# Optimization experiments

Measured on AMD Instinct MI355X. Metric: run time of the kernel, lower is better.

## Reference

```python
import jax, jax.numpy as jnp
import numpy as np

B, S, N, NODE_IN, IN_DIM, H, EMB = 2048, 168, 64, 16, 16, 64, 4
# N == H is required by the original broadcast `attention_score * station_features_emb`


def setup_inputs() -> dict:
    key = jax.random.key(0)
    ks = jax.random.split(key, 24)
    p = lambda i, shape, s=0.05: jax.random.normal(ks[i], shape, jnp.float32) * s
    inp = {
        "local_node": jax.random.normal(ks[0], (B, NODE_IN), jnp.float32),
        "station_nodes": jax.random.normal(ks[1], (B, N, NODE_IN), jnp.float32),
        "station_features": jax.random.normal(ks[2], (B, S, IN_DIM), jnp.float32),
    }
    weather = jax.random.randint(ks[3], (B, S, 1), 0, 12)
    wind = jax.random.randint(ks[4], (B, S, 1), 0, 10)
    month = jax.random.randint(ks[5], (B, S, 1), 1, 13)  # 1-indexed in source
    day = jax.random.randint(ks[6], (B, S, 1), 1, 8)
    hour = jax.random.randint(ks[7], (B, S, 1), 1, 25)
    inp["station_emb"] = jnp.stack([weather, wind, month, day, hour], axis=-1).astype(jnp.int32)  # (B,S,1,5)
    inp.update(
        emb_weather=p(8, (12, EMB), 1.0), emb_wind=p(9, (10, EMB), 1.0),
        emb_month=p(10, (12, EMB), 1.0), emb_day=p(11, (7, EMB), 1.0),
        emb_hour=p(12, (24, EMB), 1.0),
        W_nodes=p(13, (H, NODE_IN)), b_nodes=jnp.zeros((H,), jnp.float32),
        W_attn=p(14, (1, 2 * H)), b_attn=jnp.zeros((1,), jnp.float32),
        W_d1=p(15, (H // 2, IN_DIM + 5 * EMB)), b_d1=jnp.zeros((H // 2,), jnp.float32),
        W_d2=p(16, (H, H // 2)), b_d2=jnp.zeros((H,), jnp.float32),
        Wih0=p(17, (3 * H, 2 * H)), Whh0=p(18, (3 * H, H)),
        bih0=jnp.zeros((3 * H,), jnp.float32), bhh0=jnp.zeros((3 * H,), jnp.float32),
        Wih1=p(19, (3 * H, H)), Whh1=p(20, (3 * H, H)),
        bih1=jnp.zeros((3 * H,), jnp.float32), bhh1=jnp.zeros((3 * H,), jnp.float32),
        W_pred=p(21, (1, 2 * H)), b_pred=jnp.zeros((1,), jnp.float32),
    )
    return inp


def _gru_layer(x, Wih, Whh, bih, bhh):
    # x: (B,S,Din); PyTorch GRU gate math, gates ordered (r,z,n).
    xg = jnp.einsum('bsd,gd->sbg', x, Wih) + bih  # (S,B,3H) precomputed input gates
    h0 = jnp.zeros((x.shape[0], Whh.shape[1]), x.dtype)

    def step(h, xg_t):
        gh = h @ Whh.T + bhh
        xr, xz, xn = jnp.split(xg_t, 3, axis=-1)
        hr, hz, hn = jnp.split(gh, 3, axis=-1)
        r = jax.nn.sigmoid(xr + hr)
        z = jax.nn.sigmoid(xz + hz)
        n = jnp.tanh(xn + r * hn)
        h_new = (1.0 - z) * n + z * h
        return h_new, h_new

    h_last, hs = jax.lax.scan(step, h0, xg)
    return jnp.swapaxes(hs, 0, 1), h_last  # (B,S,H), (B,H)


def _forward(local_node, station_nodes, station_features, station_emb,
             emb_weather, emb_wind, emb_month, emb_day, emb_hour,
             W_nodes, b_nodes, W_attn, b_attn, W_d1, b_d1, W_d2, b_d2,
             Wih0, Whh0, bih0, bhh0, Wih1, Whh1, bih1, bhh1, W_pred, b_pred):
    local_emb = jnp.tanh(local_node @ W_nodes.T + b_nodes)          # (B,H)
    site_emb = jnp.tanh(station_nodes @ W_nodes.T + b_nodes)        # (B,N,H)
    # attn(cat(local, site)) == local@Wl + site@Ws + b, vectorized over sites
    Wl, Ws = W_attn[0, :H], W_attn[0, H:]
    energies = site_emb @ Ws + (local_emb @ Wl)[:, None] + b_attn[0]  # (B,N)
    attn = jax.nn.softmax(energies, axis=-1)                          # (B,N), N==H

    e = lambda tab, idx: tab[idx].reshape(idx.shape[0], idx.shape[1], -1)  # (B,S,EMB)
    cat = jnp.concatenate([
        station_features,
        e(emb_weather, station_emb[..., 0]),
        e(emb_wind, station_emb[..., 1]),
        e(emb_month, station_emb[..., 2] - 1),
        e(emb_day, station_emb[..., 3] - 1),
        e(emb_hour, station_emb[..., 4] - 1),
    ], axis=-1)                                                      # (B,S,IN_DIM+20)
    h1 = jnp.tanh(cat @ W_d1.T + b_d1)
    sfe = jnp.tanh(h1 @ W_d2.T + b_d2)                               # (B,S,H)

    local_feature = attn[:, None, :] * sfe                           # broadcast over seq
    features = jnp.concatenate([local_feature, sfe], axis=-1)        # (B,S,2H)

    out0, hf0 = _gru_layer(features, Wih0, Whh0, bih0, bhh0)
    out1, hf1 = _gru_layer(out0, Wih1, Whh1, bih1, bhh1)
    hidden = jnp.concatenate([hf0, hf1], axis=-1)                    # (B,2H)
    pred = jnp.tanh(hidden @ W_pred.T + b_pred)                      # (B,1)
    return pred


def reference(local_node, station_nodes, station_features, station_emb,
              emb_weather, emb_wind, emb_month, emb_day, emb_hour,
              W_nodes, b_nodes, W_attn, b_attn, W_d1, b_d1, W_d2, b_d2,
              Wih0, Whh0, bih0, bhh0, Wih1, Whh1, bih1, bhh1, W_pred, b_pred):
    return _forward(local_node, station_nodes, station_features, station_emb,
                    emb_weather, emb_wind, emb_month, emb_day, emb_hour,
                    W_nodes, b_nodes, W_attn, b_attn, W_d1, b_d1, W_d2, b_d2,
                    Wih0, Whh0, bih0, bhh0, Wih1, Whh1, bih1, bhh1, W_pred, b_pred)
```

## Files before the change

### kernel.cpp

```cpp
#include <hip/hip_runtime.h>
#include <cstdint>
#include <cstddef>

#define B_ 2048
#define S_ 168
#define NT_ 5376

typedef _Float16 h2_t __attribute__((ext_vector_type(2)));
typedef _Float16 f16x8 __attribute__((ext_vector_type(8)));
typedef float f32x4 __attribute__((ext_vector_type(4)));
typedef unsigned int u32;

__device__ __forceinline__ unsigned pack_h2f(float a, float b){
    h2_t v; v.x = (_Float16)a; v.y = (_Float16)b;
    return __builtin_bit_cast(unsigned, v);
}
__device__ __forceinline__ float fast_exp(float x){
    return __builtin_amdgcn_exp2f(x * 1.44269504088896340736f);
}
__device__ __forceinline__ float fast_sigmoid(float x){
    return __builtin_amdgcn_rcpf(1.0f + fast_exp(-x));
}
__device__ __forceinline__ float fast_tanh(float x){
    return 1.0f - 2.0f * __builtin_amdgcn_rcpf(1.0f + fast_exp(2.0f * x));
}
__device__ __forceinline__ void wsync(){
    asm volatile("s_waitcnt lgkmcnt(0)" ::: "memory");
    __builtin_amdgcn_wave_barrier();
}
__device__ __forceinline__ void bar_lds(){
    asm volatile("s_waitcnt lgkmcnt(0)\n\ts_barrier" ::: "memory");
}
__device__ __forceinline__ f32x4 mfma16(uint4 a, uint4 b, f32x4 c){
    return __builtin_amdgcn_mfma_f32_16x16x32_f16(
        __builtin_bit_cast(f16x8, a), __builtin_bit_cast(f16x8, b), c, 0, 0, 0);
}
__device__ __forceinline__ uint4 load_bfrag(const float* __restrict__ W, int ldk,
                                            int o, int kk0, int kmax){
    float w[8];
    #pragma unroll
    for (int e = 0; e < 8; ++e){
        int kk = kk0 + e;
        w[e] = (kk < kmax) ? W[o*ldk + kk] : 0.f;
    }
    uint4 r;
    r.x = pack_h2f(w[0], w[1]); r.y = pack_h2f(w[2], w[3]);
    r.z = pack_h2f(w[4], w[5]); r.w = pack_h2f(w[6], w[7]);
    return r;
}

__global__ void nbst_attn(const float* __restrict__ sn, const float* __restrict__ Wn,
                          const float* __restrict__ bn, const float* __restrict__ Wa,
                          float* __restrict__ attnO){
    __shared__ float WnL[64*16];
    __shared__ float WsL[64];
    __shared__ float bnL[64];
    const int tid = threadIdx.x;
    for (int e = tid; e < 1024; e += 256) WnL[e] = Wn[e];
    if (tid < 64){ WsL[tid] = Wa[64 + tid]; bnL[tid] = bn[tid]; }
    __syncthreads();
    const int wv = tid >> 6, l = tid & 63;
    const int b = blockIdx.x * 4 + wv;
    const float* xp = sn + ((size_t)b * 64 + l) * 16;
    float x[16];
    #pragma unroll
    for (int k = 0; k < 16; ++k) x[k] = xp[k];
    float e_i = 0.f;
    for (int h = 0; h < 64; ++h){
        float acc = bnL[h];
        #pragma unroll
        for (int k = 0; k < 16; ++k) acc += x[k] * WnL[h*16 + k];
        e_i += fast_tanh(acc) * WsL[h];
    }
    float m = e_i;
    #pragma unroll
    for (int s = 32; s >= 1; s >>= 1) m = fmaxf(m, __shfl_xor(m, s));
    float p = fast_exp(e_i - m);
    float ssum = p;
    #pragma unroll
    for (int s = 32; s >= 1; s >>= 1) ssum += __shfl_xor(ssum, s);
    attnO[(size_t)b*64 + l] = p * __builtin_amdgcn_rcpf(ssum);
}

#define A0_CAT 0
#define A0_H1  2304
#define A0_FT  3584
#define A0_WM  7936
#define A0_EMB 9984
#define A0_ATT 10244
#define A0_TOT 11268

__global__ __launch_bounds__(256, 2)
void nbst_mlpxg0(const float* __restrict__ sf, const int* __restrict__ se,
                 const float* __restrict__ e0, const float* __restrict__ e1,
                 const float* __restrict__ e2, const float* __restrict__ e3,
                 const float* __restrict__ e4,
                 const float* __restrict__ Wd1, const float* __restrict__ bd1,
                 const float* __restrict__ Wd2, const float* __restrict__ bd2,
                 const float* __restrict__ Wih0, const float* __restrict__ attnI,
                 u32* __restrict__ xg0F)
{
    __shared__ u32 sm[A0_TOT];
    float* smF = reinterpret_cast<float*>(sm);
    const int tid = threadIdx.x;
    const int w = tid >> 6, l = tid & 63;
    const int q = l >> 4, c = l & 15;

    for (int e = tid; e < 260; e += 256){
        float v;
        if (e < 48)       v = e0[e];
        else if (e < 88)  v = e1[e-48];
        else if (e < 136) v = e2[e-88];
        else if (e < 164) v = e3[e-136];
        else              v = e4[e-164];
        smF[A0_EMB + e] = v;
    }
    for (int f = w; f < 8; f += 4){
        uint4 fr;
        if (f < 4){ int n = f >> 1, ks = f & 1;
                    fr = load_bfrag(Wd1, 36, 16*n + c, 32*ks + 8*q, 36); }
        else      { int n = f - 4;
                    fr = load_bfrag(Wd2, 32, 16*n + c, 8*q, 32); }
        *reinterpret_cast<uint4*>(sm + A0_WM + (f*64 + l)*4) = fr;
    }
    uint4 bw[3][4];
    #pragma unroll
    for (int nn = 0; nn < 3; ++nn)
        #pragma unroll
        for (int ks = 0; ks < 4; ++ks)
            bw[nn][ks] = load_bfrag(Wih0, 128, 16*(w + 4*nn) + c, 32*ks + 8*q, 128);
    for (int e = tid; e < 64*18; e += 256){
        int row = e / 18, j = 18 + e % 18;
        sm[A0_CAT + row*36 + j] = 0u;
    }
    const float bb10 = bd1[c],  bb11 = bd1[16+c];
    const float bb20 = bd2[c],  bb21 = bd2[16+c];
    const float bb22 = bd2[32+c], bb23 = bd2[48+c];
    __syncthreads();

    for (int tile = blockIdx.x; tile < NT_; tile += gridDim.x){
        const int gb = tile / 42, tb = tile % 42;
        for (int e = tid; e < 1024; e += 256)
            smF[A0_ATT + e] = attnI[(size_t)(16*gb)*64 + e];
        for (int e = tid; e < 64*18; e += 256){
            int row = e / 18, j = e % 18;
            int R = (16*gb + (row & 15))*S_ + 4*tb + (row >> 4);
            float c0, c1;
            if (j < 8){
                c0 = sf[(size_t)R*16 + 2*j]; c1 = sf[(size_t)R*16 + 2*j + 1];
            } else {
                int jj = j - 8, ebl = jj >> 1, d0 = (jj & 1) * 2;
                int idx = se[(size_t)R*5 + ebl] - (ebl >= 2 ? 1 : 0);
                const int toff = (ebl==0)?0:(ebl==1)?48:(ebl==2)?88:(ebl==3)?136:164;
                c0 = smF[A0_EMB + toff + idx*4 + d0];
                c1 = smF[A0_EMB + toff + idx*4 + d0 + 1];
            }
            sm[A0_CAT + row*36 + j] = pack_h2f(c0, c1);
        }
        __syncthreads();

        {
            f32x4 c1a[2];
            c1a[0] = (f32x4){bb10, bb10, bb10, bb10};
            c1a[1] = (f32x4){bb11, bb11, bb11, bb11};
            #pragma unroll
            for (int ks = 0; ks < 2; ++ks){
                uint4 a = *reinterpret_cast<const uint4*>(
                    sm + A0_CAT + (16*w + c)*36 + ks*16 + 4*q);
                #pragma unroll
                for (int n = 0; n < 2; ++n)
                    c1a[n] = mfma16(a, *reinterpret_cast<const uint4*>(
                        sm + A0_WM + ((n*2 + ks)*64 + l)*4), c1a[n]);
            }
            #pragma unroll
            for (int n = 0; n < 2; ++n)
                #pragma unroll
                for (int j = 0; j < 4; ++j){
                    float v = fast_tanh(c1a[n][j]);
                    float vp = __shfl_xor(v, 1);
                    if (!(l & 1))
                        sm[A0_H1 + (16*w + 4*q + j)*20 + 8*n + (c >> 1)] = pack_h2f(v, vp);
                }
        }
        wsync();

        {
            uint4 a = *reinterpret_cast<const uint4*>(
                sm + A0_H1 + (16*w + c)*20 + 4*q);
            f32x4 c2[4];
            c2[0] = (f32x4){bb20, bb20, bb20, bb20};
            c2[1] = (f32x4){bb21, bb21, bb21, bb21};
            c2[2] = (f32x4){bb22, bb22, bb22, bb22};
            c2[3] = (f32x4){bb23, bb23, bb23, bb23};
            #pragma unroll
            for (int n = 0; n < 4; ++n)
                c2[n] = mfma16(a, *reinterpret_cast<const uint4*>(
                    sm + A0_WM + ((4 + n)*64 + l)*4), c2[n]);
            #pragma unroll
            for (int n = 0; n < 4; ++n)
                #pragma unroll
                for (int j = 0; j < 4; ++j){
                    float s  = fast_tanh(c2[n][j]);
                    float fa = smF[A0_ATT + (4*q + j)*64 + 16*n + c] * s;
                    float sp  = __shfl_xor(s, 1);
                    float fap = __shfl_xor(fa, 1);
                    if (!(l & 1)){
                        int row = 16*w + 4*q + j;
                        int ci = 8*n + (c >> 1);
                        sm[A0_FT + row*68 + ci]      = pack_h2f(fa, fap);
                        sm[A0_FT + row*68 + 32 + ci] = pack_h2f(s, sp);
                    }
                }
        }
        __syncthreads();

        #pragma unroll
        for (int m = 0; m < 4; ++m){
            uint4 af[4];
            #pragma unroll
            for (int ks = 0; ks < 4; ++ks)
                af[ks] = *reinterpret_cast<const uint4*>(
                    sm + A0_FT + (16*m + c)*68 + ks*16 + 4*q);
            f32x4 acc[3];
            #pragma unroll
            for (int nn = 0; nn < 3; ++nn) acc[nn] = (f32x4){0.f, 0.f, 0.f, 0.f};
            #pragma unroll
            for (int ks = 0; ks < 4; ++ks)
                #pragma unroll
                for (int nn = 0; nn < 3; ++nn)
                    acc[nn] = mfma16(af[ks], bw[nn][ks], acc[nn]);
            size_t base = ((size_t)(gb*S_ + 4*tb + m))*1536 + (size_t)w*384 + (size_t)l*6;
            uint2 s01, s23, s45;
            s01.x = pack_h2f(acc[0][0], acc[0][1]); s01.y = pack_h2f(acc[0][2], acc[0][3]);
            s23.x = pack_h2f(acc[1][0], acc[1][1]); s23.y = pack_h2f(acc[1][2], acc[1][3]);
            s45.x = pack_h2f(acc[2][0], acc[2][1]); s45.y = pack_h2f(acc[2][2], acc[2][3]);
            *reinterpret_cast<uint2*>(xg0F + base + 0) = s01;
            *reinterpret_cast<uint2*>(xg0F + base + 2) = s23;
            *reinterpret_cast<uint2*>(xg0F + base + 4) = s45;
        }
        __syncthreads();
    }
}

#define RW0 6912
#define RW1 13056
#define RHB (RW0 + RW1)
#define RF_TOT (RHB + 2048)

__global__ __launch_bounds__(512, 1)
void nbst_recf(const u32* __restrict__ xg0F,
               const float* __restrict__ Whh0,
               const float* __restrict__ bih0, const float* __restrict__ bhh0,
               const float* __restrict__ Wih1, const float* __restrict__ Whh1,
               const float* __restrict__ bih1, const float* __restrict__ bhh1,
               const float* __restrict__ Wpred, const float* __restrict__ bpred,
               float* __restrict__ outp)
{
    extern __shared__ u32 sm[];
    u32* smw0 = sm;
    u32* smw1 = sm + RW0;
    u32* HB0  = sm + RHB;
    u32* HB1  = sm + RHB + 1024;
    const int tid = threadIdx.x;
    const int w8 = tid >> 6, l = tid & 63;
    const int grp = w8 >> 2, w = w8 & 3;
    const int q = l >> 4, c = l & 15;
    const int g = blockIdx.x, B0 = g*16;

    for (int e = tid; e < 192*32; e += 512){
        int row = e >> 5, k = e & 31;
        smw0[row*36 + k] = pack_h2f(Whh0[row*64 + 2*k], Whh0[row*64 + 2*k + 1]);
    }
    for (int e = tid; e < 192*64; e += 512){
        int row = e / 64, kp = e % 64;
        smw1[row*68 + kp] = (kp < 32)
            ? pack_h2f(Wih1[row*64 + 2*kp],      Wih1[row*64 + 2*kp + 1])
            : pack_h2f(Whh1[row*64 + 2*(kp-32)], Whh1[row*64 + 2*(kp-32) + 1]);
    }
    for (int e = tid; e < 2048; e += 512) sm[RHB + e] = 0u;
    __syncthreads();

    const int gr = 16*w + c, gz = 64 + 16*w + c, gn = 128 + 16*w + c;
    const int rd0 = (c*32 + 4*q)      ^ ((c & 7) << 2);
    const int rd1 = (c*32 + 4*q + 16) ^ ((c & 7) << 2);
    int wri[4];
    #pragma unroll
    for (int j = 0; j < 4; ++j){
        int row = 4*q + j;
        wri[j] = (row*64 + 16*w + c) ^ ((row & 7) << 3);
    }

    float hv0 = 0.f, hv1 = 0.f, hv2 = 0.f, hv3 = 0.f;

    if (grp == 0){
        uint4 aBR[2], aBZ[2], aBHN[2];
        #pragma unroll
        for (int ks = 0; ks < 2; ++ks){
            aBR[ks]  = *reinterpret_cast<const uint4*>(smw0 + gr*36 + 16*ks + 4*q);
            aBZ[ks]  = *reinterpret_cast<const uint4*>(smw0 + gz*36 + 16*ks + 4*q);
            aBHN[ks] = *reinterpret_cast<const uint4*>(smw0 + gn*36 + 16*ks + 4*q);
        }
        const float br0 = bih0[gr] + bhh0[gr], bz0 = bih0[gz] + bhh0[gz];
        const float bxn0 = bih0[gn], bhn0 = bhh0[gn];

        const u32* xb = xg0F + (size_t)g * S_ * 1536 + (size_t)w * 384 + (size_t)l * 6;
        uint2 x0a, x0b, x0c, x1a, x1b, x1c, x2a, x2b, x2c, x3a, x3b, x3c;
        {
            const u32* p0 = xb;
            const u32* p1 = xb + 1536;
            const u32* p2 = xb + 2*1536;
            const u32* p3 = xb + 3*1536;
            x0a = *(const uint2*)(p0+0); x0b = *(const uint2*)(p0+2); x0c = *(const uint2*)(p0+4);
            x1a = *(const uint2*)(p1+0); x1b = *(const uint2*)(p1+2); x1c = *(const uint2*)(p1+4);
            x2a = *(const uint2*)(p2+0); x2b = *(const uint2*)(p2+2); x2c = *(const uint2*)(p2+4);
            x3a = *(const uint2*)(p3+0); x3b = *(const uint2*)(p3+2); x3c = *(const uint2*)(p3+4);
        }

#define L0STEP(I, XA, XB, XC) do{                                               \
    const int i_ = (I);                                                         \
    const u32* hp0_ = HB0 + ((i_ + 1) & 1) * 512;                               \
    uint4 hA0a_ = *(const uint4*)(hp0_ + rd0);                                  \
    uint4 hA0b_ = *(const uint4*)(hp0_ + rd1);                                  \
    f32x4 aRh_ = {br0,br0,br0,br0};                                             \
    f32x4 aZh_ = {bz0,bz0,bz0,bz0};                                             \
    f32x4 aHN_ = {bhn0,bhn0,bhn0,bhn0};                                         \
    aRh_ = mfma16(hA0a_, aBR[0], aRh_);  aRh_ = mfma16(hA0b_, aBR[1], aRh_);    \
    aZh_ = mfma16(hA0a_, aBZ[0], aZh_);  aZh_ = mfma16(hA0b_, aBZ[1], aZh_);    \
    aHN_ = mfma16(hA0a_, aBHN[0], aHN_); aHN_ = mfma16(hA0b_, aBHN[1], aHN_);   \
    h2_t xR01_ = __builtin_bit_cast(h2_t, (XA).x);                              \
    h2_t xR23_ = __builtin_bit_cast(h2_t, (XA).y);                              \
    h2_t xZ01_ = __builtin_bit_cast(h2_t, (XB).x);                              \
    h2_t xZ23_ = __builtin_bit_cast(h2_t, (XB).y);                              \
    h2_t xN01_ = __builtin_bit_cast(h2_t, (XC).x);                              \
    h2_t xN23_ = __builtin_bit_cast(h2_t, (XC).y);                              \
    _Float16* hw_ = (_Float16*)(HB0 + (i_ & 1) * 512);                          \
    float rg_, zg_, ng_;                                                        \
    rg_ = fast_sigmoid((float)xR01_.x + aRh_[0]);                               \
    zg_ = fast_sigmoid((float)xZ01_.x + aZh_[0]);                               \
    ng_ = fast_tanh((float)xN01_.x + bxn0 + rg_*aHN_[0]);                       \
    hv0 = (1.f - zg_)*ng_ + zg_*hv0; hw_[wri[0]] = (_Float16)hv0;               \
    rg_ = fast_sigmoid((float)xR01_.y + aRh_[1]);                               \
    zg_ = fast_sigmoid((float)xZ01_.y + aZh_[1]);                               \
    ng_ = fast_tanh((float)xN01_.y + bxn0 + rg_*aHN_[1]);                       \
    hv1 = (1.f - zg_)*ng_ + zg_*hv1; hw_[wri[1]] = (_Float16)hv1;               \
    rg_ = fast_sigmoid((float)xR23_.x + aRh_[2]);                               \
    zg_ = fast_sigmoid((float)xZ23_.x + aZh_[2]);                               \
    ng_ = fast_tanh((float)xN23_.x + bxn0 + rg_*aHN_[2]);                       \
    hv2 = (1.f - zg_)*ng_ + zg_*hv2; hw_[wri[2]] = (_Float16)hv2;               \
    rg_ = fast_sigmoid((float)xR23_.y + aRh_[3]);                               \
    zg_ = fast_sigmoid((float)xZ23_.y + aZh_[3]);                               \
    ng_ = fast_tanh((float)xN23_.y + bxn0 + rg_*aHN_[3]);                       \
    hv3 = (1.f - zg_)*ng_ + zg_*hv3; hw_[wri[3]] = (_Float16)hv3;               \
    {   int tn_ = (i_ + 4 < S_) ? i_ + 4 : S_ - 1;                              \
        const u32* xp_ = xb + (size_t)tn_ * 1536;                               \
        (XA) = *(const uint2*)(xp_ + 0);                                        \
        (XB) = *(const uint2*)(xp_ + 2);                                        \
        (XC) = *(const uint2*)(xp_ + 4);                                        \
    }                                                                           \
    bar_lds();                                                                  \
} while(0)

        L0STEP(0, x0a, x0b, x0c);
        L0STEP(1, x1a, x1b, x1c);
        L0STEP(2, x2a, x2b, x2c);
        L0STEP(3, x3a, x3b, x3c);
        #pragma unroll 1
        for (int i4 = 1; i4 < 42; ++i4){
            const int ib = 4*i4;
            L0STEP(ib + 0, x0a, x0b, x0c);
            L0STEP(ib + 1, x1a, x1b, x1c);
            L0STEP(ib + 2, x2a, x2b, x2c);
            L0STEP(ib + 3, x3a, x3b, x3c);
        }
        bar_lds();
#undef L0STEP
    } else {
        uint4 xBR[2], xBZ[2], xBXN[2], hBR[2], hBZ[2], hBHN[2];
        #pragma unroll
        for (int ks = 0; ks < 2; ++ks){
            xBR[ks] = *reinterpret_cast<const uint4*>(smw1 + gr*68 + 16*ks + 4*q);
            xBZ[ks] = *reinterpret_cast<const uint4*>(smw1 + gz*68 + 16*ks + 4*q);
            hBR[ks] = *reinterpret_cast<const uint4*>(smw1 + gr*68 + 32 + 16*ks + 4*q);
            hBZ[ks] = *reinterpret_cast<const uint4*>(smw1 + gz*68 + 32 + 16*ks + 4*q);
        }
        xBXN[0] = *reinterpret_cast<const uint4*>(smw1 + gn*68 +      4*q);
        xBXN[1] = *reinterpret_cast<const uint4*>(smw1 + gn*68 + 16 + 4*q);
        hBHN[0] = *reinterpret_cast<const uint4*>(smw1 + gn*68 + 32 + 4*q);
        hBHN[1] = *reinterpret_cast<const uint4*>(smw1 + gn*68 + 48 + 4*q);
        const float br1 = bih1[gr] + bhh1[gr], bz1 = bih1[gz] + bhh1[gz];
        const float bxn1 = bih1[gn], bhn1 = bhh1[gn];

        bar_lds();
        #pragma unroll 1
        for (int i = 1; i <= S_; ++i){
            const u32* hp0_ = HB0 + ((i + 1) & 1) * 512;
            const u32* hp1_ = HB1 + ((i + 1) & 1) * 512;
            uint4 hA0a_ = *(const uint4*)(hp0_ + rd0);
            uint4 hA0b_ = *(const uint4*)(hp0_ + rd1);
            uint4 hA1a_ = *(const uint4*)(hp1_ + rd0);
            uint4 hA1b_ = *(const uint4*)(hp1_ + rd1);
            f32x4 cR_  = {br1,br1,br1,br1};
            f32x4 cZ_  = {bz1,bz1,bz1,bz1};
            f32x4 cXN_ = {bxn1,bxn1,bxn1,bxn1};
            f32x4 cHN_ = {bhn1,bhn1,bhn1,bhn1};
            cR_  = mfma16(hA0a_, xBR[0], cR_);   cR_  = mfma16(hA0b_, xBR[1], cR_);
            cZ_  = mfma16(hA0a_, xBZ[0], cZ_);   cZ_  = mfma16(hA0b_, xBZ[1], cZ_);
            cXN_ = mfma16(hA0a_, xBXN[0], cXN_); cXN_ = mfma16(hA0b_, xBXN[1], cXN_);
            cR_  = mfma16(hA1a_, hBR[0], cR_);   cR_  = mfma16(hA1b_, hBR[1], cR_);
            cZ_  = mfma16(hA1a_, hBZ[0], cZ_);   cZ_  = mfma16(hA1b_, hBZ[1], cZ_);
            cHN_ = mfma16(hA1a_, hBHN[0], cHN_); cHN_ = mfma16(hA1b_, hBHN[1], cHN_);
            _Float16* hw_ = (_Float16*)(HB1 + (i & 1) * 512);
            float rg_, zg_, ng_;
            rg_ = fast_sigmoid(cR_[0]); zg_ = fast_sigmoid(cZ_[0]);
            ng_ = fast_tanh(cXN_[0] + rg_*cHN_[0]);
            hv0 = (1.f - zg_)*ng_ + zg_*hv0; hw_[wri[0]] = (_Float16)hv0;
            rg_ = fast_sigmoid(cR_[1]); zg_ = fast_sigmoid(cZ_[1]);
            ng_ = fast_tanh(cXN_[1] + rg_*cHN_[1]);
            hv1 = (1.f - zg_)*ng_ + zg_*hv1; hw_[wri[1]] = (_Float16)hv1;
            rg_ = fast_sigmoid(cR_[2]); zg_ = fast_sigmoid(cZ_[2]);
            ng_ = fast_tanh(cXN_[2] + rg_*cHN_[2]);
            hv2 = (1.f - zg_)*ng_ + zg_*hv2; hw_[wri[2]] = (_Float16)hv2;
            rg_ = fast_sigmoid(cR_[3]); zg_ = fast_sigmoid(cZ_[3]);
            ng_ = fast_tanh(cXN_[3] + rg_*cHN_[3]);
            hv3 = (1.f - zg_)*ng_ + zg_*hv3; hw_[wri[3]] = (_Float16)hv3;
            bar_lds();
        }
    }

    __syncthreads();
    float* s0 = reinterpret_cast<float*>(sm);
    float* s1 = reinterpret_cast<float*>(sm) + 1024;
    {
        float* sd = (grp == 0) ? s0 : s1;
        #pragma unroll
        for (int j = 0; j < 4; ++j){
            int row = 4*q + j;
            float hv = (j == 0) ? hv0 : (j == 1) ? hv1 : (j == 2) ? hv2 : hv3;
            sd[row*64 + 16*w + c] = hv;
        }
    }
    __syncthreads();
    if (tid < 256){
        const int r = tid >> 4, cg = tid & 15;
        const float* hp0 = s0 + r*64 + 4*cg;
        const float* hp1 = s1 + r*64 + 4*cg;
        const float* wp0 = Wpred + 4*cg;
        const float* wp1 = Wpred + 64 + 4*cg;
        float part = hp0[0]*wp0[0] + hp0[1]*wp0[1] + hp0[2]*wp0[2] + hp0[3]*wp0[3]
                   + hp1[0]*wp1[0] + hp1[1]*wp1[1] + hp1[2]*wp1[2] + hp1[3]*wp1[3];
        part += __shfl_xor(part, 8);
        part += __shfl_xor(part, 4);
        part += __shfl_xor(part, 2);
        part += __shfl_xor(part, 1);
        if (cg == 0) outp[B0 + r] = fast_tanh(part + bpred[0]);
    }
}

extern "C" void kernel_launch(void* const* d_in, const int* in_sizes, int n_in,
                              void* d_out, int out_size, void* d_ws, size_t ws_size,
                              hipStream_t stream) {
    (void)in_sizes; (void)n_in; (void)out_size; (void)ws_size;
    const float* station_nodes    = (const float*)d_in[1];
    const float* station_features = (const float*)d_in[2];
    const int*   station_emb      = (const int*)d_in[3];
    const float* e0 = (const float*)d_in[4];
    const float* e1 = (const float*)d_in[5];
    const float* e2 = (const float*)d_in[6];
    const float* e3 = (const float*)d_in[7];
    const float* e4 = (const float*)d_in[8];
    const float* W_nodes = (const float*)d_in[9];
    const float* b_nodes = (const float*)d_in[10];
    const float* W_attn  = (const float*)d_in[11];
    const float* W_d1 = (const float*)d_in[13];
    const float* b_d1 = (const float*)d_in[14];
    const float* W_d2 = (const float*)d_in[15];
    const float* b_d2 = (const float*)d_in[16];
    const float* Wih0 = (const float*)d_in[17];
    const float* Whh0 = (const float*)d_in[18];
    const float* bih0 = (const float*)d_in[19];
    const float* bhh0 = (const float*)d_in[20];
    const float* Wih1 = (const float*)d_in[21];
    const float* Whh1 = (const float*)d_in[22];
    const float* bih1 = (const float*)d_in[23];
    const float* bhh1 = (const float*)d_in[24];
    const float* W_pred = (const float*)d_in[25];
    const float* b_pred = (const float*)d_in[26];
    float* outp = (float*)d_out;

    char* ws = (char*)d_ws;
    float* attnW = (float*)ws;
    u32*   xg0F  = (u32*)(ws + (1u<<20));

    hipFuncSetAttribute((const void*)nbst_recf,
                        hipFuncAttributeMaxDynamicSharedMemorySize, 96*1024);

    nbst_attn<<<dim3(512), dim3(256), 0, stream>>>(station_nodes, W_nodes, b_nodes, W_attn, attnW);
    nbst_mlpxg0<<<dim3(768), dim3(256), 0, stream>>>(
        station_features, station_emb, e0, e1, e2, e3, e4,
        W_d1, b_d1, W_d2, b_d2, Wih0, attnW, xg0F);
    nbst_recf<<<dim3(128), dim3(512), RF_TOT*4, stream>>>(
        xg0F, Whh0, bih0, bhh0, Wih1, Whh1, bih1, bhh1,
        W_pred, b_pred, outp);
}
```

Before: 190.1 us.

## Split GRU recurrence into 4-row batch groups across 512 blocks

The recurrent kernel now processes 4 batch rows per block instead of 16, launching 512 blocks so more compute units run the serial time loop. Weight fragments are loaded straight from global memory into registers rather than staged in LDS, shrinking shared memory to the hidden-state buffers. The xg0 producer writes a per-batch-row layout to match. Only a quarter of each MFMA tile carries real rows, so compute per step is wasted, and block count may exceed one wave of resident blocks.

```diff
diff --git a/kernel.cpp b/kernel.cpp
--- a/kernel.cpp
+++ b/kernel.cpp
@@ -5,6 +5,7 @@
 #define B_ 2048
 #define S_ 168
 #define NT_ 5376
+#define NG_ 512
 
 typedef _Float16 h2_t __attribute__((ext_vector_type(2)));
 typedef _Float16 f16x8 __attribute__((ext_vector_type(8)));
@@ -98,7 +99,7 @@
                  const float* __restrict__ Wd1, const float* __restrict__ bd1,
                  const float* __restrict__ Wd2, const float* __restrict__ bd2,
                  const float* __restrict__ Wih0, const float* __restrict__ attnI,
-                 u32* __restrict__ xg0F)
+                 u32* __restrict__ xgG)
 {
     __shared__ u32 sm[A0_TOT];
     float* smF = reinterpret_cast<float*>(sm);
@@ -229,26 +230,24 @@
                 #pragma unroll
                 for (int nn = 0; nn < 3; ++nn)
                     acc[nn] = mfma16(af[ks], bw[nn][ks], acc[nn]);
-            size_t base = ((size_t)(gb*S_ + 4*tb + m))*1536 + (size_t)w*384 + (size_t)l*6;
-            uint2 s01, s23, s45;
-            s01.x = pack_h2f(acc[0][0], acc[0][1]); s01.y = pack_h2f(acc[0][2], acc[0][3]);
-            s23.x = pack_h2f(acc[1][0], acc[1][1]); s23.y = pack_h2f(acc[1][2], acc[1][3]);
-            s45.x = pack_h2f(acc[2][0], acc[2][1]); s45.y = pack_h2f(acc[2][2], acc[2][3]);
-            *reinterpret_cast<uint2*>(xg0F + base + 0) = s01;
-            *reinterpret_cast<uint2*>(xg0F + base + 2) = s23;
-            *reinterpret_cast<uint2*>(xg0F + base + 4) = s45;
+            const int t = 4*tb + m;
+            const size_t gbase = ((size_t)(4*gb + q) * S_ + t) * 384;
+            #pragma unroll
+            for (int nn = 0; nn < 3; ++nn){
+                uint2 s2;
+                s2.x = pack_h2f(acc[nn][0], acc[nn][1]);
+                s2.y = pack_h2f(acc[nn][2], acc[nn][3]);
+                *reinterpret_cast<uint2*>(xgG + gbase + (16*(w + 4*nn) + c)*2) = s2;
+            }
         }
         __syncthreads();
     }
 }
 
-#define RW0 6912
-#define RW1 13056
-#define RHB (RW0 + RW1)
-#define RF_TOT (RHB + 2048)
+#define RF_TOT 2048
 
 __global__ __launch_bounds__(512, 1)
-void nbst_recf(const u32* __restrict__ xg0F,
+void nbst_recf(const u32* __restrict__ xgG,
                const float* __restrict__ Whh0,
                const float* __restrict__ bih0, const float* __restrict__ bhh0,
                const float* __restrict__ Wih1, const float* __restrict__ Whh1,
@@ -256,29 +255,16 @@
                const float* __restrict__ Wpred, const float* __restrict__ bpred,
                float* __restrict__ outp)
 {
-    extern __shared__ u32 sm[];
-    u32* smw0 = sm;
-    u32* smw1 = sm + RW0;
-    u32* HB0  = sm + RHB;
-    u32* HB1  = sm + RHB + 1024;
+    __shared__ u32 sm[RF_TOT];
+    u32* HB0 = sm;
+    u32* HB1 = sm + 1024;
     const int tid = threadIdx.x;
     const int w8 = tid >> 6, l = tid & 63;
     const int grp = w8 >> 2, w = w8 & 3;
     const int q = l >> 4, c = l & 15;
-    const int g = blockIdx.x, B0 = g*16;
-
-    for (int e = tid; e < 192*32; e += 512){
-        int row = e >> 5, k = e & 31;
-        smw0[row*36 + k] = pack_h2f(Whh0[row*64 + 2*k], Whh0[row*64 + 2*k + 1]);
-    }
-    for (int e = tid; e < 192*64; e += 512){
-        int row = e / 64, kp = e % 64;
-        smw1[row*68 + kp] = (kp < 32)
-            ? pack_h2f(Wih1[row*64 + 2*kp],      Wih1[row*64 + 2*kp + 1])
-            : pack_h2f(Whh1[row*64 + 2*(kp-32)], Whh1[row*64 + 2*(kp-32) + 1]);
-    }
-    for (int e = tid; e < 2048; e += 512) sm[RHB + e] = 0u;
-    __syncthreads();
+    const int g = blockIdx.x;
+
+    for (int e = tid; e < 2048; e += 512) sm[e] = 0u;
 
     const int gr = 16*w + c, gz = 64 + 16*w + c, gn = 128 + 16*w + c;
     const int rd0 = (c*32 + 4*q)      ^ ((c & 7) << 2);
@@ -291,29 +277,30 @@
     }
 
     float hv0 = 0.f, hv1 = 0.f, hv2 = 0.f, hv3 = 0.f;
+    __syncthreads();
 
     if (grp == 0){
         uint4 aBR[2], aBZ[2], aBHN[2];
         #pragma unroll
         for (int ks = 0; ks < 2; ++ks){
-            aBR[ks]  = *reinterpret_cast<const uint4*>(smw0 + gr*36 + 16*ks + 4*q);
-            aBZ[ks]  = *reinterpret_cast<const uint4*>(smw0 + gz*36 + 16*ks + 4*q);
-            aBHN[ks] = *reinterpret_cast<const uint4*>(smw0 + gn*36 + 16*ks + 4*q);
+            aBR[ks]  = load_bfrag(Whh0, 64, gr, 32*ks + 8*q, 64);
+            aBZ[ks]  = load_bfrag(Whh0, 64, gz, 32*ks + 8*q, 64);
+            aBHN[ks] = load_bfrag(Whh0, 64, gn, 32*ks + 8*q, 64);
         }
         const float br0 = bih0[gr] + bhh0[gr], bz0 = bih0[gz] + bhh0[gz];
         const float bxn0 = bih0[gn], bhn0 = bhh0[gn];
 
-        const u32* xb = xg0F + (size_t)g * S_ * 1536 + (size_t)w * 384 + (size_t)l * 6;
+        const u32* xb = xgG + (size_t)g * S_ * 384 + (16*w + c)*2;
         uint2 x0a, x0b, x0c, x1a, x1b, x1c, x2a, x2b, x2c, x3a, x3b, x3c;
-        {
+        if (q == 0){
             const u32* p0 = xb;
-            const u32* p1 = xb + 1536;
-            const u32* p2 = xb + 2*1536;
-            const u32* p3 = xb + 3*1536;
-            x0a = *(const uint2*)(p0+0); x0b = *(const uint2*)(p0+2); x0c = *(const uint2*)(p0+4);
-            x1a = *(const uint2*)(p1+0); x1b = *(const uint2*)(p1+2); x1c = *(const uint2*)(p1+4);
-            x2a = *(const uint2*)(p2+0); x2b = *(const uint2*)(p2+2); x2c = *(const uint2*)(p2+4);
-            x3a = *(const uint2*)(p3+0); x3b = *(const uint2*)(p3+2); x3c = *(const uint2*)(p3+4);
+            const u32* p1 = xb + 384;
+            const u32* p2 = xb + 2*384;
+            const u32* p3 = xb + 3*384;
+            x0a = *(const uint2*)(p0+0); x0b = *(const uint2*)(p0+128); x0c = *(const uint2*)(p0+256);
+            x1a = *(const uint2*)(p1+0); x1b = *(const uint2*)(p1+128); x1c = *(const uint2*)(p1+256);
+            x2a = *(const uint2*)(p2+0); x2b = *(const uint2*)(p2+128); x2c = *(const uint2*)(p2+256);
+            x3a = *(const uint2*)(p3+0); x3b = *(const uint2*)(p3+128); x3c = *(const uint2*)(p3+256);
         }
 
 #define L0STEP(I, XA, XB, XC) do{                                               \
@@ -327,35 +314,36 @@
     aRh_ = mfma16(hA0a_, aBR[0], aRh_);  aRh_ = mfma16(hA0b_, aBR[1], aRh_);    \
     aZh_ = mfma16(hA0a_, aBZ[0], aZh_);  aZh_ = mfma16(hA0b_, aBZ[1], aZh_);    \
     aHN_ = mfma16(hA0a_, aBHN[0], aHN_); aHN_ = mfma16(hA0b_, aBHN[1], aHN_);   \
-    h2_t xR01_ = __builtin_bit_cast(h2_t, (XA).x);                              \
-    h2_t xR23_ = __builtin_bit_cast(h2_t, (XA).y);                              \
-    h2_t xZ01_ = __builtin_bit_cast(h2_t, (XB).x);                              \
-    h2_t xZ23_ = __builtin_bit_cast(h2_t, (XB).y);                              \
-    h2_t xN01_ = __builtin_bit_cast(h2_t, (XC).x);                              \
-    h2_t xN23_ = __builtin_bit_cast(h2_t, (XC).y);                              \
-    _Float16* hw_ = (_Float16*)(HB0 + (i_ & 1) * 512);                          \
-    float rg_, zg_, ng_;                                                        \
-    rg_ = fast_sigmoid((float)xR01_.x + aRh_[0]);                               \
-    zg_ = fast_sigmoid((float)xZ01_.x + aZh_[0]);                               \
-    ng_ = fast_tanh((float)xN01_.x + bxn0 + rg_*aHN_[0]);                       \
-    hv0 = (1.f - zg_)*ng_ + zg_*hv0; hw_[wri[0]] = (_Float16)hv0;               \
-    rg_ = fast_sigmoid((float)xR01_.y + aRh_[1]);                               \
-    zg_ = fast_sigmoid((float)xZ01_.y + aZh_[1]);                               \
-    ng_ = fast_tanh((float)xN01_.y + bxn0 + rg_*aHN_[1]);                       \
-    hv1 = (1.f - zg_)*ng_ + zg_*hv1; hw_[wri[1]] = (_Float16)hv1;               \
-    rg_ = fast_sigmoid((float)xR23_.x + aRh_[2]);                               \
-    zg_ = fast_sigmoid((float)xZ23_.x + aZh_[2]);                               \
-    ng_ = fast_tanh((float)xN23_.x + bxn0 + rg_*aHN_[2]);                       \
-    hv2 = (1.f - zg_)*ng_ + zg_*hv2; hw_[wri[2]] = (_Float16)hv2;               \
-    rg_ = fast_sigmoid((float)xR23_.y + aRh_[3]);                               \
-    zg_ = fast_sigmoid((float)xZ23_.y + aZh_[3]);                               \
-    ng_ = fast_tanh((float)xN23_.y + bxn0 + rg_*aHN_[3]);                       \
-    hv3 = (1.f - zg_)*ng_ + zg_*hv3; hw_[wri[3]] = (_Float16)hv3;               \
-    {   int tn_ = (i_ + 4 < S_) ? i_ + 4 : S_ - 1;                              \
-        const u32* xp_ = xb + (size_t)tn_ * 1536;                               \
+    if (q == 0){                                                                \
+        h2_t xR01_ = __builtin_bit_cast(h2_t, (XA).x);                          \
+        h2_t xR23_ = __builtin_bit_cast(h2_t, (XA).y);                          \
+        h2_t xZ01_ = __builtin_bit_cast(h2_t, (XB).x);                          \
+        h2_t xZ23_ = __builtin_bit_cast(h2_t, (XB).y);                          \
+        h2_t xN01_ = __builtin_bit_cast(h2_t, (XC).x);                          \
+        h2_t xN23_ = __builtin_bit_cast(h2_t, (XC).y);                          \
+        _Float16* hw_ = (_Float16*)(HB0 + (i_ & 1) * 512);                      \
+        float rg_, zg_, ng_;                                                    \
+        rg_ = fast_sigmoid((float)xR01_.x + aRh_[0]);                           \
+        zg_ = fast_sigmoid((float)xZ01_.x + aZh_[0]);                           \
+        ng_ = fast_tanh((float)xN01_.x + bxn0 + rg_*aHN_[0]);                   \
+        hv0 = (1.f - zg_)*ng_ + zg_*hv0; hw_[wri[0]] = (_Float16)hv0;           \
+        rg_ = fast_sigmoid((float)xR01_.y + aRh_[1]);                           \
+        zg_ = fast_sigmoid((float)xZ01_.y + aZh_[1]);                           \
+        ng_ = fast_tanh((float)xN01_.y + bxn0 + rg_*aHN_[1]);                   \
+        hv1 = (1.f - zg_)*ng_ + zg_*hv1; hw_[wri[1]] = (_Float16)hv1;           \
+        rg_ = fast_sigmoid((float)xR23_.x + aRh_[2]);                           \
+        zg_ = fast_sigmoid((float)xZ23_.x + aZh_[2]);                           \
+        ng_ = fast_tanh((float)xN23_.x + bxn0 + rg_*aHN_[2]);                   \
+        hv2 = (1.f - zg_)*ng_ + zg_*hv2; hw_[wri[2]] = (_Float16)hv2;           \
+        rg_ = fast_sigmoid((float)xR23_.y + aRh_[3]);                           \
+        zg_ = fast_sigmoid((float)xZ23_.y + aZh_[3]);                           \
+        ng_ = fast_tanh((float)xN23_.y + bxn0 + rg_*aHN_[3]);                   \
+        hv3 = (1.f - zg_)*ng_ + zg_*hv3; hw_[wri[3]] = (_Float16)hv3;           \
+        int tn_ = (i_ + 4 < S_) ? i_ + 4 : S_ - 1;                              \
+        const u32* xp_ = xb + (size_t)tn_ * 384;                                \
         (XA) = *(const uint2*)(xp_ + 0);                                        \
-        (XB) = *(const uint2*)(xp_ + 2);                                        \
-        (XC) = *(const uint2*)(xp_ + 4);                                        \
+        (XB) = *(const uint2*)(xp_ + 128);                                      \
+        (XC) = *(const uint2*)(xp_ + 256);                                      \
     }                                                                           \
     bar_lds();                                                                  \
 } while(0)
@@ -378,15 +366,13 @@
         uint4 xBR[2], xBZ[2], xBXN[2], hBR[2], hBZ[2], hBHN[2];
         #pragma unroll
         for (int ks = 0; ks < 2; ++ks){
-            xBR[ks] = *reinterpret_cast<const uint4*>(smw1 + gr*68 + 16*ks + 4*q);
-            xBZ[ks] = *reinterpret_cast<const uint4*>(smw1 + gz*68 + 16*ks + 4*q);
-            hBR[ks] = *reinterpret_cast<const uint4*>(smw1 + gr*68 + 32 + 16*ks + 4*q);
-            hBZ[ks] = *reinterpret_cast<const uint4*>(smw1 + gz*68 + 32 + 16*ks + 4*q);
-        }
-        xBXN[0] = *reinterpret_cast<const uint4*>(smw1 + gn*68 +      4*q);
-        xBXN[1] = *reinterpret_cast<const uint4*>(smw1 + gn*68 + 16 + 4*q);
-        hBHN[0] = *reinterpret_cast<const uint4*>(smw1 + gn*68 + 32 + 4*q);
-        hBHN[1] = *reinterpret_cast<const uint4*>(smw1 + gn*68 + 48 + 4*q);
+            xBR[ks]  = load_bfrag(Wih1, 64, gr, 32*ks + 8*q, 64);
+            xBZ[ks]  = load_bfrag(Wih1, 64, gz, 32*ks + 8*q, 64);
+            xBXN[ks] = load_bfrag(Wih1, 64, gn, 32*ks + 8*q, 64);
+            hBR[ks]  = load_bfrag(Whh1, 64, gr, 32*ks + 8*q, 64);
+            hBZ[ks]  = load_bfrag(Whh1, 64, gz, 32*ks + 8*q, 64);
+            hBHN[ks] = load_bfrag(Whh1, 64, gn, 32*ks + 8*q, 64);
+        }
         const float br1 = bih1[gr] + bhh1[gr], bz1 = bih1[gz] + bhh1[gz];
         const float bxn1 = bih1[gn], bhn1 = bhh1[gn];
 
@@ -409,38 +395,39 @@
             cR_  = mfma16(hA1a_, hBR[0], cR_);   cR_  = mfma16(hA1b_, hBR[1], cR_);
             cZ_  = mfma16(hA1a_, hBZ[0], cZ_);   cZ_  = mfma16(hA1b_, hBZ[1], cZ_);
             cHN_ = mfma16(hA1a_, hBHN[0], cHN_); cHN_ = mfma16(hA1b_, hBHN[1], cHN_);
-            _Float16* hw_ = (_Float16*)(HB1 + (i & 1) * 512);
-            float rg_, zg_, ng_;
-            rg_ = fast_sigmoid(cR_[0]); zg_ = fast_sigmoid(cZ_[0]);
-            ng_ = fast_tanh(cXN_[0] + rg_*cHN_[0]);
-            hv0 = (1.f - zg_)*ng_ + zg_*hv0; hw_[wri[0]] = (_Float16)hv0;
-            rg_ = fast_sigmoid(cR_[1]); zg_ = fast_sigmoid(cZ_[1]);
-            ng_ = fast_tanh(cXN_[1] + rg_*cHN_[1]);
-            hv1 = (1.f - zg_)*ng_ + zg_*hv1; hw_[wri[1]] = (_Float16)hv1;
-            rg_ = fast_sigmoid(cR_[2]); zg_ = fast_sigmoid(cZ_[2]);
-            ng_ = fast_tanh(cXN_[2] + rg_*cHN_[2]);
-            hv2 = (1.f - zg_)*ng_ + zg_*hv2; hw_[wri[2]] = (_Float16)hv2;
-            rg_ = fast_sigmoid(cR_[3]); zg_ = fast_sigmoid(cZ_[3]);
-            ng_ = fast_tanh(cXN_[3] + rg_*cHN_[3]);
-            hv3 = (1.f - zg_)*ng_ + zg_*hv3; hw_[wri[3]] = (_Float16)hv3;
+            if (q == 0){
+                _Float16* hw_ = (_Float16*)(HB1 + (i & 1) * 512);
+                float rg_, zg_, ng_;
+                rg_ = fast_sigmoid(cR_[0]); zg_ = fast_sigmoid(cZ_[0]);
+                ng_ = fast_tanh(cXN_[0] + rg_*cHN_[0]);
+                hv0 = (1.f - zg_)*ng_ + zg_*hv0; hw_[wri[0]] = (_Float16)hv0;
+                rg_ = fast_sigmoid(cR_[1]); zg_ = fast_sigmoid(cZ_[1]);
+                ng_ = fast_tanh(cXN_[1] + rg_*cHN_[1]);
+                hv1 = (1.f - zg_)*ng_ + zg_*hv1; hw_[wri[1]] = (_Float16)hv1;
+                rg_ = fast_sigmoid(cR_[2]); zg_ = fast_sigmoid(cZ_[2]);
+                ng_ = fast_tanh(cXN_[2] + rg_*cHN_[2]);
+                hv2 = (1.f - zg_)*ng_ + zg_*hv2; hw_[wri[2]] = (_Float16)hv2;
+                rg_ = fast_sigmoid(cR_[3]); zg_ = fast_sigmoid(cZ_[3]);
+                ng_ = fast_tanh(cXN_[3] + rg_*cHN_[3]);
+                hv3 = (1.f - zg_)*ng_ + zg_*hv3; hw_[wri[3]] = (_Float16)hv3;
+            }
             bar_lds();
         }
     }
 
     __syncthreads();
     float* s0 = reinterpret_cast<float*>(sm);
-    float* s1 = reinterpret_cast<float*>(sm) + 1024;
-    {
+    float* s1 = reinterpret_cast<float*>(sm) + 256;
+    if (q == 0){
         float* sd = (grp == 0) ? s0 : s1;
         #pragma unroll
         for (int j = 0; j < 4; ++j){
-            int row = 4*q + j;
             float hv = (j == 0) ? hv0 : (j == 1) ? hv1 : (j == 2) ? hv2 : hv3;
-            sd[row*64 + 16*w + c] = hv;
+            sd[j*64 + 16*w + c] = hv;
         }
     }
     __syncthreads();
-    if (tid < 256){
+    if (tid < 64){
         const int r = tid >> 4, cg = tid & 15;
         const float* hp0 = s0 + r*64 + 4*cg;
         const float* hp1 = s1 + r*64 + 4*cg;
@@ -452,7 +439,7 @@
         part += __shfl_xor(part, 4);
         part += __shfl_xor(part, 2);
         part += __shfl_xor(part, 1);
-        if (cg == 0) outp[B0 + r] = fast_tanh(part + bpred[0]);
+        if (cg == 0) outp[g*4 + r] = fast_tanh(part + bpred[0]);
     }
 }
 
@@ -489,16 +476,13 @@
 
     char* ws = (char*)d_ws;
     float* attnW = (float*)ws;
-    u32*   xg0F  = (u32*)(ws + (1u<<20));
-
-    hipFuncSetAttribute((const void*)nbst_recf,
-                        hipFuncAttributeMaxDynamicSharedMemorySize, 96*1024);
+    u32*   xgG   = (u32*)(ws + (1u<<20));
 
     nbst_attn<<<dim3(512), dim3(256), 0, stream>>>(station_nodes, W_nodes, b_nodes, W_attn, attnW);
     nbst_mlpxg0<<<dim3(768), dim3(256), 0, stream>>>(
         station_features, station_emb, e0, e1, e2, e3, e4,
-        W_d1, b_d1, W_d2, b_d2, Wih0, attnW, xg0F);
-    nbst_recf<<<dim3(128), dim3(512), RF_TOT*4, stream>>>(
-        xg0F, Whh0, bih0, bhh0, Wih1, Whh1, bih1, bhh1,
+        W_d1, b_d1, W_d2, b_d2, Wih0, attnW, xgG);
+    nbst_recf<<<dim3(NG_), dim3(512), 0, stream>>>(
+        xgG, Whh0, bih0, bhh0, Wih1, Whh1, bih1, bhh1,
         W_pred, b_pred, outp);
 }
```

Result: slower. 252.0 us (+32.6%).
